# Optimization experiments

Measured on AMD Instinct MI355X. Metric: run time of the kernel, lower is better.

Reference implementation:

```python
import jax, jax.numpy as jnp
import numpy as np

B, N, M, C1, C2 = 4, 8192, 2048, 128, 256
H1, H2 = 256, 128  # mlp = [C2+C1, 256, 128]
EPS_DIST = 1e-8
EPS_BN = 1e-5
K = 3


def setup_inputs() -> dict:
    key = jax.random.key(0)
    ks = jax.random.split(key, 6)
    return {
        "unknown": jax.random.normal(ks[0], (B, N, 3), dtype=jnp.float32),
        "known": jax.random.normal(ks[1], (B, M, 3), dtype=jnp.float32),
        "unknow_feats": jax.random.normal(ks[2], (B, C1, N), dtype=jnp.float32),
        "known_feats": jax.random.normal(ks[3], (B, C2, M), dtype=jnp.float32),
        "W1": jax.random.normal(ks[4], (H1, C1 + C2), dtype=jnp.float32) * 0.05,
        "g1": jnp.ones((H1,), jnp.float32),
        "b1": jnp.zeros((H1,), jnp.float32),
        "W2": jax.random.normal(ks[5], (H2, H1), dtype=jnp.float32) * 0.05,
        "g2": jnp.ones((H2,), jnp.float32),
        "b2": jnp.zeros((H2,), jnp.float32),
    }


def _bn_relu(x, g, b):
    # training-mode BatchNorm over (batch, spatial) axes for (B, C, N) tensor
    mean = jnp.mean(x, axis=(0, 2), keepdims=True)
    var = jnp.var(x, axis=(0, 2), keepdims=True)
    y = (x - mean) * jax.lax.rsqrt(var + EPS_BN) * g[None, :, None] + b[None, :, None]
    return jax.nn.relu(y)


def reference(unknown, known, unknow_feats, known_feats, W1, g1, b1, W2, g2, b2):
    # 3-NN: squared euclidean distances (B, N, M) via expansion (avoids B,N,M,3 temp)
    d2 = (
        jnp.sum(unknown * unknown, axis=-1)[:, :, None]
        + jnp.sum(known * known, axis=-1)[:, None, :]
        - 2.0 * jnp.einsum("bnc,bmc->bnm", unknown, known)
    )
    neg_d, idx = jax.lax.top_k(-d2, K)  # smallest-K squared dists
    dist = -neg_d  # (B, N, K), squared distances (pytorch3d knn_points convention)
    recip = 1.0 / (dist + EPS_DIST)
    weight = recip / jnp.sum(recip, axis=2, keepdims=True)  # (B, N, K)

    kf = jnp.swapaxes(known_feats, 1, 2)  # (B, M, C2)
    grouped = jax.vmap(lambda f, i: f[i])(kf, idx)  # (B, N, K, C2)
    interp = jnp.einsum("bnkc,bnk->bcn", grouped, weight)  # (B, C2, N)

    x = jnp.concatenate([interp, unknow_feats], axis=1)  # (B, C2+C1, N)
    x = _bn_relu(jnp.einsum("oc,bcn->bon", W1, x), g1, b1)
    x = _bn_relu(jnp.einsum("oc,bcn->bon", W2, x), g2, b2)
    return x  # (B, H2, N)
```

## Files before the change

kernel.cpp:

```cpp
#include <hip/hip_runtime.h>
#include <hip/hip_bf16.h>
#include <cstdint>
#include <cstddef>

typedef unsigned short u16;
typedef __attribute__((ext_vector_type(8))) short bf16x8;
typedef __attribute__((ext_vector_type(4))) float f32x4;

constexpr int Bn = 4;
constexpr int Nq = 8192;
constexpr int Mk = 2048;
constexpr int C1c = 128;
constexpr int C2c = 256;
constexpr int H1c = 256;
constexpr int H2c = 128;

__device__ __forceinline__ float bf2f(u16 u) {
    union { uint32_t i; float f; } v;
    v.i = (uint32_t)u << 16;
    return v.f;
}
__device__ __forceinline__ u16 f2bf(float f) {
    const uint32_t x = __float_as_uint(f);
    return (u16)((x + 0x7FFFu + ((x >> 16) & 1u)) >> 16);
}
__device__ __forceinline__ uint32_t cvtpk(float lo, float hi) {
    uint32_t r;
    asm("v_cvt_pk_bf16_f32 %0, %1, %2" : "=v"(r) : "v"(lo), "v"(hi));
    return r;
}

__global__ __launch_bounds__(256) void knn_prep_kernel(
    const float* __restrict__ W1, const float* __restrict__ W2,
    u16* __restrict__ W1b, u16* __restrict__ W2b,
    const float* __restrict__ KF, u16* __restrict__ KFt,
    const float* __restrict__ UF, u16* __restrict__ UFt,
    const float* __restrict__ unknown, const float* __restrict__ known,
    int* __restrict__ idx_out, float* __restrict__ w_out)
{
    __shared__ __align__(16) char smem[32768];
    const int bid = blockIdx.x;
    const int t = threadIdx.x;

    if (bid < 2048) {
        float4* kp = (float4*)smem;
        const int b = bid >> 9;
        const int n0 = (bid & 511) * 16;

        const float* kb = known + (size_t)b * Mk * 3;
        for (int i = t; i < Mk; i += 256) {
            const float x = kb[i * 3 + 0], y = kb[i * 3 + 1], z = kb[i * 3 + 2];
            kp[i] = make_float4(x, y, z, fmaf(x, x, fmaf(y, y, z * z)));
        }
        __syncthreads();

        const int q = n0 + (t >> 4);
        const int s = t & 15;
        const float* u = unknown + ((size_t)b * Nq + q) * 3;
        const float ux = u[0], uy = u[1], uz = u[2];
        const float nux = -2.0f * ux, nuy = -2.0f * uy, nuz = -2.0f * uz;
        const float uu = fmaf(ux, ux, fmaf(uy, uy, uz * uz));

        float d0 = 1e30f, d1 = 1e30f, d2 = 1e30f;
        int i0 = 0, i1 = 0, i2 = 0;

        auto ins = [&](float d, int i) {
            const bool c0 = d < d0, c1 = d < d1, c2 = d < d2;
            const float nd0 = fminf(d0, d);
            const float nd1 = __builtin_amdgcn_fmed3f(d0, d, d1);
            const float nd2 = __builtin_amdgcn_fmed3f(d1, d, d2);
            i2 = c1 ? i1 : (c2 ? i : i2);
            i1 = c0 ? i0 : (c1 ? i : i1);
            i0 = c0 ? i : i0;
            d0 = nd0; d1 = nd1; d2 = nd2;
        };

        #pragma unroll 8
        for (int it = 0; it < Mk / 16; ++it) {
            const int m = it * 16 + s;
            const float4 p = kp[m];
            const float d = fmaf(nux, p.x, fmaf(nuy, p.y, fmaf(nuz, p.z, p.w)));
            ins(d, m);
        }
        #pragma unroll
        for (int off = 1; off <= 8; off <<= 1) {
            const float e0 = __shfl_xor(d0, off), e1 = __shfl_xor(d1, off), e2 = __shfl_xor(d2, off);
            const int j0 = __shfl_xor(i0, off), j1 = __shfl_xor(i1, off), j2 = __shfl_xor(i2, off);
            ins(e0, j0);
            ins(e1, j1);
            ins(e2, j2);
        }
        if (s == 0) {
            const float f0 = d0 + uu, f1 = d1 + uu, f2 = d2 + uu;
            const float r0 = 1.0f / (f0 + 1e-8f);
            const float r1 = 1.0f / (f1 + 1e-8f);
            const float r2 = 1.0f / (f2 + 1e-8f);
            const float inv = 1.0f / (r0 + r1 + r2);
            const size_t base = ((size_t)b * Nq + q) * 3;
            idx_out[base + 0] = i0;
            idx_out[base + 1] = i1;
            idx_out[base + 2] = i2;
            w_out[base + 0] = r0 * inv;
            w_out[base + 1] = r1 * inv;
            w_out[base + 2] = r2 * inv;
        }
    } else if (bid < 2176) {
        const int cb = bid - 2048;
        const float* X = (cb < 96) ? W1 : W2;
        u16* Y = (cb < 96) ? W1b : W2b;
        const int i = ((cb < 96) ? cb : (cb - 96)) * 256 + t;
        const float4 v = *(const float4*)&X[(size_t)i * 4];
        ushort4 o;
        o.x = f2bf(v.x); o.y = f2bf(v.y); o.z = f2bf(v.z); o.w = f2bf(v.w);
        *(ushort4*)&Y[(size_t)i * 4] = o;
    } else {
        const float* X;
        u16* Y;
        int C, M, m0, c0;
        if (bid < 2688) {
            const int f = bid - 2176;
            const int b = f >> 7, rem = f & 127;
            C = C2c; M = Mk; m0 = (rem >> 2) * 64; c0 = (rem & 3) * 64;
            X = KF + (size_t)b * C * M;
            Y = KFt + (size_t)b * M * C;
        } else {
            const int f = bid - 2688;
            const int b = f >> 8, rem = f & 255;
            C = C1c; M = Nq; m0 = (rem >> 1) * 64; c0 = (rem & 1) * 64;
            X = UF + (size_t)b * C * M;
            Y = UFt + (size_t)b * M * C;
        }
        float (*T)[65] = (float(*)[65])smem;
        const int m4 = (t & 15) * 4, cr = t >> 4;
        #pragma unroll
        for (int i = 0; i < 4; ++i) {
            const float4 v = *(const float4*)&X[(size_t)(c0 + cr + i * 16) * M + m0 + m4];
            T[cr + i * 16][m4 + 0] = v.x;
            T[cr + i * 16][m4 + 1] = v.y;
            T[cr + i * 16][m4 + 2] = v.z;
            T[cr + i * 16][m4 + 3] = v.w;
        }
        __syncthreads();
        const int c4 = (t & 15) * 4, mr = t >> 4;
        #pragma unroll
        for (int i = 0; i < 4; ++i) {
            const int m = mr + i * 16;
            ushort4 o;
            o.x = f2bf(T[c4 + 0][m]);
            o.y = f2bf(T[c4 + 1][m]);
            o.z = f2bf(T[c4 + 2][m]);
            o.w = f2bf(T[c4 + 3][m]);
            *(ushort4*)&Y[(size_t)(m0 + m) * C + c0 + c4] = o;
        }
    }
}

__device__ __forceinline__ uint4 bnx(uint4 x, const float* scs, const float* bis, int k) {
    const u16* p = (const u16*)&x;
    const float4 s0 = *(const float4*)&scs[k];
    const float4 s1 = *(const float4*)&scs[k + 4];
    const float4 b0 = *(const float4*)&bis[k];
    const float4 b1 = *(const float4*)&bis[k + 4];
    const float* sa = (const float*)&s0;
    const float* sb = (const float*)&s1;
    const float* ba = (const float*)&b0;
    const float* bb = (const float*)&b1;
    uint4 o;
    uint32_t* po = (uint32_t*)&o;
    #pragma unroll
    for (int w2 = 0; w2 < 2; ++w2) {
        const float a0 = fmaxf(0.0f, fmaf(bf2f(p[2 * w2 + 0]), sa[2 * w2 + 0], ba[2 * w2 + 0]));
        const float a1 = fmaxf(0.0f, fmaf(bf2f(p[2 * w2 + 1]), sa[2 * w2 + 1], ba[2 * w2 + 1]));
        po[w2] = cvtpk(a0, a1);
    }
    #pragma unroll
    for (int w2 = 0; w2 < 2; ++w2) {
        const float a0 = fmaxf(0.0f, fmaf(bf2f(p[4 + 2 * w2 + 0]), sb[2 * w2 + 0], bb[2 * w2 + 0]));
        const float a1 = fmaxf(0.0f, fmaf(bf2f(p[4 + 2 * w2 + 1]), sb[2 * w2 + 1], bb[2 * w2 + 1]));
        po[2 + w2] = cvtpk(a0, a1);
    }
    return o;
}

template <int GATHER, int OUT_BF16, int STATS, int BNIN>
__global__ __launch_bounds__(256) void mfma_gemm(
    const u16* __restrict__ A, int lda, size_t sA,
    const u16* __restrict__ Bt, int ldb, size_t sB,
    void* __restrict__ Cout, int ldc, size_t sC,
    int nK,
    const u16* __restrict__ Ptb,
    const int* __restrict__ idx, const float* __restrict__ wgt, int nrows,
    const float* __restrict__ bn_s, const float* __restrict__ bn_b,
    float* __restrict__ partS, float* __restrict__ partQ)
{
    __shared__ u16 As[4096];
    __shared__ u16 Bs[4096];
    __shared__ float scs[256], bis[256];
    __shared__ float sS[2][128], sQ[2][128];

    const int b = blockIdx.z;
    const int m0 = blockIdx.x * 128, n0 = blockIdx.y * 128;
    const int t = threadIdx.x;
    const int l = t & 63, wv = t >> 6;
    const int wr = wv >> 1, wc = wv & 1;

    if (BNIN) {
        scs[t] = bn_s[t];
        bis[t] = bn_b[t];
    }

    const u16* Ab = A + (size_t)b * sA;
    const u16* Btb = Bt + (size_t)b * sB;
    const int rA0 = t >> 2, rA1 = (t + 256) >> 2;
    const int ko = (t & 3) * 8;

    f32x4 acc[4][4];
    const f32x4 z = {0.0f, 0.0f, 0.0f, 0.0f};
    #pragma unroll
    for (int i = 0; i < 4; ++i)
        #pragma unroll
        for (int j = 0; j < 4; ++j) acc[i][j] = z;

    uint4 a0 = *(const uint4*)&Ab[(size_t)(m0 + rA0) * lda + ko];
    uint4 a1 = *(const uint4*)&Ab[(size_t)(m0 + rA1) * lda + ko];
    uint4 b0 = *(const uint4*)&Btb[(size_t)(n0 + rA0) * ldb + ko];
    uint4 b1 = *(const uint4*)&Btb[(size_t)(n0 + rA1) * ldb + ko];
    if (BNIN) __syncthreads();

    for (int kt = 0; kt < nK; ++kt) {
        *(uint4*)&As[t * 8] = a0;
        *(uint4*)&As[(t + 256) * 8] = a1;
        if (BNIN) {
            const int k = kt * 32 + ko;
            *(uint4*)&Bs[t * 8] = bnx(b0, scs, bis, k);
            *(uint4*)&Bs[(t + 256) * 8] = bnx(b1, scs, bis, k);
        } else {
            *(uint4*)&Bs[t * 8] = b0;
            *(uint4*)&Bs[(t + 256) * 8] = b1;
        }
        __syncthreads();
        if (kt + 1 < nK) {
            const int k0 = (kt + 1) * 32;
            a0 = *(const uint4*)&Ab[(size_t)(m0 + rA0) * lda + k0 + ko];
            a1 = *(const uint4*)&Ab[(size_t)(m0 + rA1) * lda + k0 + ko];
            b0 = *(const uint4*)&Btb[(size_t)(n0 + rA0) * ldb + k0 + ko];
            b1 = *(const uint4*)&Btb[(size_t)(n0 + rA1) * ldb + k0 + ko];
        }
        bf16x8 af[4], bf[4];
        #pragma unroll
        for (int f = 0; f < 4; ++f) {
            af[f] = *(const bf16x8*)&As[(wr * 64 + f * 16 + (l & 15)) * 32 + (l >> 4) * 8];
            bf[f] = *(const bf16x8*)&Bs[(wc * 64 + f * 16 + (l & 15)) * 32 + (l >> 4) * 8];
        }
        #pragma unroll
        for (int i = 0; i < 4; ++i)
            #pragma unroll
            for (int j = 0; j < 4; ++j)
                acc[i][j] = __builtin_amdgcn_mfma_f32_16x16x32_bf16(af[i], bf[j], acc[i][j], 0, 0, 0);
        __syncthreads();
    }

    const int cb = l & 15;
    const int rg = (l >> 4) * 4;
    float sj[4] = {0, 0, 0, 0}, qj[4] = {0, 0, 0, 0};
    #pragma unroll
    for (int i = 0; i < 4; ++i) {
        #pragma unroll
        for (int r = 0; r < 4; ++r) {
            const int R = m0 + wr * 64 + i * 16 + rg + r;
            const u16 *P0 = nullptr, *P1 = nullptr, *P2 = nullptr;
            float w0 = 0.0f, w1 = 0.0f, w2 = 0.0f;
            if (GATHER) {
                const size_t ib = ((size_t)b * nrows + R) * 3;
                const int j0 = idx[ib], j1 = idx[ib + 1], j2 = idx[ib + 2];
                w0 = wgt[ib];
                w1 = wgt[ib + 1];
                w2 = wgt[ib + 2];
                const u16* Pb = Ptb + (size_t)b * Mk * 256;
                P0 = Pb + (size_t)j0 * 256;
                P1 = Pb + (size_t)j1 * 256;
                P2 = Pb + (size_t)j2 * 256;
            }
            #pragma unroll
            for (int j = 0; j < 4; ++j) {
                const int Cc = n0 + wc * 64 + j * 16 + cb;
                float v = acc[i][j][r];
                if (GATHER)
                    v += w0 * bf2f(P0[Cc]) + w1 * bf2f(P1[Cc]) + w2 * bf2f(P2[Cc]);
                if (OUT_BF16)
                    ((u16*)Cout)[(size_t)b * sC + (size_t)R * ldc + Cc] = f2bf(v);
                else
                    ((float*)Cout)[(size_t)b * sC + (size_t)R * ldc + Cc] = v;
                if (STATS == 1) {
                    sj[j] += v;
                    qj[j] += v * v;
                }
                if (STATS == 2) acc[i][j][r] = v;
            }
        }
    }

    if (STATS == 1) {
        #pragma unroll
        for (int j = 0; j < 4; ++j) {
            float s = sj[j], q = qj[j];
            s += __shfl_xor(s, 16); s += __shfl_xor(s, 32);
            q += __shfl_xor(q, 16); q += __shfl_xor(q, 32);
            if (l < 16) {
                sS[wr][wc * 64 + j * 16 + l] = s;
                sQ[wr][wc * 64 + j * 16 + l] = q;
            }
        }
        __syncthreads();
        if (t < 128) {
            const float S = sS[0][t] + sS[1][t];
            const float Q = sQ[0][t] + sQ[1][t];
            const int pblk = blockIdx.z * gridDim.x + blockIdx.x;
            partS[(size_t)pblk * 256 + blockIdx.y * 128 + t] = S;
            partQ[(size_t)pblk * 256 + blockIdx.y * 128 + t] = Q;
        }
    }
    if (STATS == 2) {
        #pragma unroll
        for (int i = 0; i < 4; ++i) {
            #pragma unroll
            for (int r = 0; r < 4; ++r) {
                float s = acc[i][0][r] + acc[i][1][r] + acc[i][2][r] + acc[i][3][r];
                float q = acc[i][0][r] * acc[i][0][r] + acc[i][1][r] * acc[i][1][r] +
                          acc[i][2][r] * acc[i][2][r] + acc[i][3][r] * acc[i][3][r];
                s += __shfl_xor(s, 1); s += __shfl_xor(s, 2);
                s += __shfl_xor(s, 4); s += __shfl_xor(s, 8);
                q += __shfl_xor(q, 1); q += __shfl_xor(q, 2);
                q += __shfl_xor(q, 4); q += __shfl_xor(q, 8);
                if ((l & 15) == 0) {
                    const int row = wr * 64 + i * 16 + (l >> 4) * 4 + r;
                    sS[wc][row] = s;
                    sQ[wc][row] = q;
                }
            }
        }
        __syncthreads();
        if (t < 128) {
            const float S = sS[0][t] + sS[1][t];
            const float Q = sQ[0][t] + sQ[1][t];
            const int pblk = blockIdx.z * gridDim.y + blockIdx.y;
            partS[(size_t)pblk * 128 + t] = S;
            partQ[(size_t)pblk * 128 + t] = Q;
        }
    }
}

__global__ __launch_bounds__(1024) void bn_finalize(
    const float* __restrict__ pS, const float* __restrict__ pQ,
    const float* __restrict__ g, const float* __restrict__ beta,
    float* __restrict__ scale, float* __restrict__ bias,
    int C, int np, float cnt)
{
    __shared__ float rs[1024], rq[1024];
    const int t = threadIdx.x;
    const int c = t & (C - 1);
    const int sl = t / C;
    const int nsl = 1024 / C;
    float s = 0.0f, q = 0.0f;
    for (int i = sl; i < np; i += nsl) {
        s += pS[(size_t)i * C + c];
        q += pQ[(size_t)i * C + c];
    }
    rs[t] = s;
    rq[t] = q;
    __syncthreads();
    if (t < C) {
        for (int k = 1; k < nsl; ++k) {
            s += rs[t + k * C];
            q += rq[t + k * C];
        }
        const float mean = s / cnt;
        const float var = q / cnt - mean * mean;
        const float r = rsqrtf(var + 1e-5f);
        const float sc = g[t] * r;
        scale[t] = sc;
        bias[t] = beta[t] - mean * sc;
    }
}

__global__ __launch_bounds__(256) void bn2_apply_kernel(
    float* __restrict__ Y,
    const float* __restrict__ pS, const float* __restrict__ pQ,
    const float* __restrict__ g, const float* __restrict__ beta)
{
    __shared__ float rs[256], rq[256];
    const int t = threadIdx.x;
    const size_t base = (size_t)blockIdx.x * 1024;
    const int c = (int)((base / Nq) % H2c);

    rs[t] = pS[(size_t)t * 128 + c];
    rq[t] = pQ[(size_t)t * 128 + c];
    __syncthreads();
    for (int off = 128; off > 0; off >>= 1) {
        if (t < off) {
            rs[t] += rs[t + off];
            rq[t] += rq[t + off];
        }
        __syncthreads();
    }
    if (t == 0) {
        const float cnt = (float)(Bn * Nq);
        const float mean = rs[0] / cnt;
        const float var = rq[0] / cnt - mean * mean;
        const float r = rsqrtf(var + 1e-5f);
        const float sc = g[c] * r;
        rs[0] = sc;
        rq[0] = beta[c] - mean * sc;
    }
    __syncthreads();
    const float sc = rs[0], bi = rq[0];
    float4 v = *(float4*)&Y[base + t * 4];
    v.x = fmaxf(0.0f, fmaf(v.x, sc, bi));
    v.y = fmaxf(0.0f, fmaf(v.y, sc, bi));
    v.z = fmaxf(0.0f, fmaf(v.z, sc, bi));
    v.w = fmaxf(0.0f, fmaf(v.w, sc, bi));
    *(float4*)&Y[base + t * 4] = v;
}

extern "C" void kernel_launch(void* const* d_in, const int* in_sizes, int n_in,
                              void* d_out, int out_size, void* d_ws, size_t ws_size,
                              hipStream_t stream) {
    const float* unknown = (const float*)d_in[0];
    const float* known = (const float*)d_in[1];
    const float* unknow_feats = (const float*)d_in[2];
    const float* known_feats = (const float*)d_in[3];
    const float* W1 = (const float*)d_in[4];
    const float* g1 = (const float*)d_in[5];
    const float* b1 = (const float*)d_in[6];
    const float* W2 = (const float*)d_in[7];
    const float* g2 = (const float*)d_in[8];
    const float* b2 = (const float*)d_in[9];
    float* out = (float*)d_out;

    char* w = (char*)d_ws;
    u16* KFt = (u16*)w; w += (size_t)Bn * Mk * C2c * 2;
    u16* UFt = (u16*)w; w += (size_t)Bn * Nq * C1c * 2;
    u16* W1b = (u16*)w; w += (size_t)H1c * 384 * 2;
    u16* W2b = (u16*)w; w += (size_t)H2c * H1c * 2;
    u16* Ptb = (u16*)w; w += (size_t)Bn * Mk * H1c * 2;
    u16* y1b = (u16*)w; w += (size_t)Bn * Nq * H1c * 2;
    int* idx = (int*)w; w += (size_t)Bn * Nq * 3 * 4;
    float* wgt = (float*)w; w += (size_t)Bn * Nq * 3 * 4;
    float* pS1 = (float*)w; w += (size_t)256 * 256 * 4;
    float* pQ1 = (float*)w; w += (size_t)256 * 256 * 4;
    float* pS2 = (float*)w; w += (size_t)256 * 128 * 4;
    float* pQ2 = (float*)w; w += (size_t)256 * 128 * 4;
    float* scale1 = (float*)w; w += 1024;
    float* bias1 = (float*)w; w += 1024;

    knn_prep_kernel<<<3712, 256, 0, stream>>>(W1, W2, W1b, W2b,
                                              known_feats, KFt, unknow_feats, UFt,
                                              unknown, known, idx, wgt);

    mfma_gemm<0, 1, 0, 0><<<dim3(Mk / 128, H1c / 128, Bn), 256, 0, stream>>>(
        KFt, C2c, (size_t)Mk * C2c,
        W1b, 384, 0,
        Ptb, H1c, (size_t)Mk * H1c,
        C2c / 32, nullptr, nullptr, nullptr, 0,
        nullptr, nullptr, nullptr, nullptr);

    mfma_gemm<1, 1, 1, 0><<<dim3(Nq / 128, H1c / 128, Bn), 256, 0, stream>>>(
        UFt, C1c, (size_t)Nq * C1c,
        W1b + C2c, 384, 0,
        y1b, H1c, (size_t)Nq * H1c,
        C1c / 32, Ptb, idx, wgt, Nq,
        nullptr, nullptr, pS1, pQ1);

    bn_finalize<<<1, 1024, 0, stream>>>(pS1, pQ1, g1, b1, scale1, bias1,
                                        H1c, 256, (float)(Bn * Nq));

    mfma_gemm<0, 0, 2, 1><<<dim3(1, Nq / 128, Bn), 256, 0, stream>>>(
        W2b, H1c, 0,
        y1b, H1c, (size_t)Nq * H1c,
        out, Nq, (size_t)H2c * Nq,
        H1c / 32, nullptr, nullptr, nullptr, 0,
        scale1, bias1, pS2, pQ2);

    bn2_apply_kernel<<<(Bn * H2c * Nq) / 1024, 256, 0, stream>>>(out, pS2, pQ2, g2, b2);
}
```

Before: 109.2 us.

## Fuse known-feature projection into prep kernel, pair-split KNN scan, split GEMM3 tiles

The known_feats transpose plus separate MFMA GEMM for the W1 projection is replaced by an FP32 SIMT tiled GEMM inside the prep kernel, which writes Ptb directly and removes one launch and the KFt buffer. The KNN scan now handles two candidates per iteration, sorting the pair first and inserting the larger one with a cheaper partial insert; the shuffle merge also uses reduced insert variants. The templated GEMM is split into specialised kernels, and the final GEMM uses 64-row tiles over a grid twice as large for more parallelism. The FP32 SIMT projection is slower per flop than MFMA and may lengthen the prep kernel's critical path.

```diff
diff --git a/kernel.cpp b/kernel.cpp
--- a/kernel.cpp
+++ b/kernel.cpp
@@ -33,7 +33,7 @@
 __global__ __launch_bounds__(256) void knn_prep_kernel(
     const float* __restrict__ W1, const float* __restrict__ W2,
     u16* __restrict__ W1b, u16* __restrict__ W2b,
-    const float* __restrict__ KF, u16* __restrict__ KFt,
+    const float* __restrict__ KF, u16* __restrict__ Ptb,
     const float* __restrict__ UF, u16* __restrict__ UFt,
     const float* __restrict__ unknown, const float* __restrict__ known,
     int* __restrict__ idx_out, float* __restrict__ w_out)
@@ -74,21 +74,41 @@
             i0 = c0 ? i : i0;
             d0 = nd0; d1 = nd1; d2 = nd2;
         };
-
-        #pragma unroll 8
-        for (int it = 0; it < Mk / 16; ++it) {
-            const int m = it * 16 + s;
-            const float4 p = kp[m];
-            const float d = fmaf(nux, p.x, fmaf(nuy, p.y, fmaf(nuz, p.z, p.w)));
-            ins(d, m);
+        auto ins_hi = [&](float d, int i) {
+            const bool c1 = d < d1, c2 = d < d2;
+            const float nd1 = fminf(d1, d);
+            const float nd2 = __builtin_amdgcn_fmed3f(d1, d, d2);
+            i2 = c1 ? i1 : (c2 ? i : i2);
+            i1 = c1 ? i : i1;
+            d1 = nd1; d2 = nd2;
+        };
+        auto ins_top = [&](float d, int i) {
+            const bool c2 = d < d2;
+            d2 = fminf(d2, d);
+            i2 = c2 ? i : i2;
+        };
+
+        #pragma unroll 4
+        for (int it = 0; it < Mk / 32; ++it) {
+            const int ma = it * 16 + s;
+            const int mb = ma + 1024;
+            const float4 pa = kp[ma];
+            const float4 pb = kp[mb];
+            const float da = fmaf(nux, pa.x, fmaf(nuy, pa.y, fmaf(nuz, pa.z, pa.w)));
+            const float db = fmaf(nux, pb.x, fmaf(nuy, pb.y, fmaf(nuz, pb.z, pb.w)));
+            const bool cab = da < db;
+            const float dlo = fminf(da, db), dhi = fmaxf(da, db);
+            const int ilo = cab ? ma : mb, ihi = cab ? mb : ma;
+            ins(dlo, ilo);
+            ins_hi(dhi, ihi);
         }
         #pragma unroll
         for (int off = 1; off <= 8; off <<= 1) {
             const float e0 = __shfl_xor(d0, off), e1 = __shfl_xor(d1, off), e2 = __shfl_xor(d2, off);
             const int j0 = __shfl_xor(i0, off), j1 = __shfl_xor(i1, off), j2 = __shfl_xor(i2, off);
             ins(e0, j0);
-            ins(e1, j1);
-            ins(e2, j2);
+            ins_hi(e1, j1);
+            ins_top(e2, j2);
         }
         if (s == 0) {
             const float f0 = d0 + uu, f1 = d1 + uu, f2 = d2 + uu;
@@ -104,8 +124,59 @@
             w_out[base + 1] = r1 * inv;
             w_out[base + 2] = r2 * inv;
         }
-    } else if (bid < 2176) {
-        const int cb = bid - 2048;
+    } else if (bid < 2304) {
+        float (*Xs)[128] = (float(*)[128])smem;
+        float (*Ws)[65] = (float(*)[65])(smem + 8192);
+        const int f = bid - 2048;
+        const int b = f >> 6;
+        const int rem = f & 63;
+        const int m0 = (rem >> 2) * 128;
+        const int h0 = (rem & 3) * 64;
+        const float* Xb = KF + (size_t)b * C2c * Mk;
+        const int tx = t & 15, ty = t >> 4;
+
+        float acc[8][4] = {};
+        for (int k0 = 0; k0 < C2c; k0 += 16) {
+            {
+                const int mx = (t & 31) * 4, kx = t >> 5;
+                #pragma unroll
+                for (int i = 0; i < 2; ++i)
+                    *(float4*)&Xs[kx + i * 8][mx] =
+                        *(const float4*)&Xb[(size_t)(k0 + kx + i * 8) * Mk + m0 + mx];
+            }
+            {
+                const int kw = t & 15, hw = t >> 4;
+                #pragma unroll
+                for (int i = 0; i < 4; ++i)
+                    Ws[kw][hw + i * 16] = W1[(size_t)(h0 + hw + i * 16) * 384 + k0 + kw];
+            }
+            __syncthreads();
+            #pragma unroll
+            for (int k = 0; k < 16; ++k) {
+                float a[8], bv[4];
+                *(float4*)&a[0] = *(const float4*)&Xs[k][ty * 8];
+                *(float4*)&a[4] = *(const float4*)&Xs[k][ty * 8 + 4];
+                *(float4*)&bv[0] = *(const float4*)&Ws[k][tx * 4];
+                #pragma unroll
+                for (int i = 0; i < 8; ++i)
+                    #pragma unroll
+                    for (int j = 0; j < 4; ++j)
+                        acc[i][j] = fmaf(a[i], bv[j], acc[i][j]);
+            }
+            __syncthreads();
+        }
+        u16* Yb = Ptb + (size_t)b * Mk * 256;
+        #pragma unroll
+        for (int i = 0; i < 8; ++i) {
+            ushort4 o;
+            o.x = f2bf(acc[i][0]);
+            o.y = f2bf(acc[i][1]);
+            o.z = f2bf(acc[i][2]);
+            o.w = f2bf(acc[i][3]);
+            *(ushort4*)&Yb[(size_t)(m0 + ty * 8 + i) * 256 + h0 + tx * 4] = o;
+        }
+    } else if (bid < 2432) {
+        const int cb = bid - 2304;
         const float* X = (cb < 96) ? W1 : W2;
         u16* Y = (cb < 96) ? W1b : W2b;
         const int i = ((cb < 96) ? cb : (cb - 96)) * 256 + t;
@@ -114,27 +185,16 @@
         o.x = f2bf(v.x); o.y = f2bf(v.y); o.z = f2bf(v.z); o.w = f2bf(v.w);
         *(ushort4*)&Y[(size_t)i * 4] = o;
     } else {
-        const float* X;
-        u16* Y;
-        int C, M, m0, c0;
-        if (bid < 2688) {
-            const int f = bid - 2176;
-            const int b = f >> 7, rem = f & 127;
-            C = C2c; M = Mk; m0 = (rem >> 2) * 64; c0 = (rem & 3) * 64;
-            X = KF + (size_t)b * C * M;
-            Y = KFt + (size_t)b * M * C;
-        } else {
-            const int f = bid - 2688;
-            const int b = f >> 8, rem = f & 255;
-            C = C1c; M = Nq; m0 = (rem >> 1) * 64; c0 = (rem & 1) * 64;
-            X = UF + (size_t)b * C * M;
-            Y = UFt + (size_t)b * M * C;
-        }
+        const int f = bid - 2432;
+        const int b = f >> 8, rem = f & 255;
+        const int m0 = (rem >> 1) * 64, c0 = (rem & 1) * 64;
+        const float* X = UF + (size_t)b * C1c * Nq;
+        u16* Y = UFt + (size_t)b * Nq * C1c;
         float (*T)[65] = (float(*)[65])smem;
         const int m4 = (t & 15) * 4, cr = t >> 4;
         #pragma unroll
         for (int i = 0; i < 4; ++i) {
-            const float4 v = *(const float4*)&X[(size_t)(c0 + cr + i * 16) * M + m0 + m4];
+            const float4 v = *(const float4*)&X[(size_t)(c0 + cr + i * 16) * Nq + m0 + m4];
             T[cr + i * 16][m4 + 0] = v.x;
             T[cr + i * 16][m4 + 1] = v.y;
             T[cr + i * 16][m4 + 2] = v.z;
@@ -150,7 +210,7 @@
             o.y = f2bf(T[c4 + 1][m]);
             o.z = f2bf(T[c4 + 2][m]);
             o.w = f2bf(T[c4 + 3][m]);
-            *(ushort4*)&Y[(size_t)(m0 + m) * C + c0 + c4] = o;
+            *(ushort4*)&Y[(size_t)(m0 + m) * C1c + c0 + c4] = o;
         }
     }
 }
@@ -182,20 +242,17 @@
     return o;
 }
 
-template <int GATHER, int OUT_BF16, int STATS, int BNIN>
-__global__ __launch_bounds__(256) void mfma_gemm(
+__global__ __launch_bounds__(256) void mfma_gemm2(
     const u16* __restrict__ A, int lda, size_t sA,
-    const u16* __restrict__ Bt, int ldb, size_t sB,
-    void* __restrict__ Cout, int ldc, size_t sC,
+    const u16* __restrict__ Bt, int ldb,
+    u16* __restrict__ Cout,
     int nK,
     const u16* __restrict__ Ptb,
-    const int* __restrict__ idx, const float* __restrict__ wgt, int nrows,
-    const float* __restrict__ bn_s, const float* __restrict__ bn_b,
+    const int* __restrict__ idx, const float* __restrict__ wgt,
     float* __restrict__ partS, float* __restrict__ partQ)
 {
     __shared__ u16 As[4096];
     __shared__ u16 Bs[4096];
-    __shared__ float scs[256], bis[256];
     __shared__ float sS[2][128], sQ[2][128];
 
     const int b = blockIdx.z;
@@ -204,13 +261,7 @@
     const int l = t & 63, wv = t >> 6;
     const int wr = wv >> 1, wc = wv & 1;
 
-    if (BNIN) {
-        scs[t] = bn_s[t];
-        bis[t] = bn_b[t];
-    }
-
     const u16* Ab = A + (size_t)b * sA;
-    const u16* Btb = Bt + (size_t)b * sB;
     const int rA0 = t >> 2, rA1 = (t + 256) >> 2;
     const int ko = (t & 3) * 8;
 
@@ -223,28 +274,21 @@
 
     uint4 a0 = *(const uint4*)&Ab[(size_t)(m0 + rA0) * lda + ko];
     uint4 a1 = *(const uint4*)&Ab[(size_t)(m0 + rA1) * lda + ko];
-    uint4 b0 = *(const uint4*)&Btb[(size_t)(n0 + rA0) * ldb + ko];
-    uint4 b1 = *(const uint4*)&Btb[(size_t)(n0 + rA1) * ldb + ko];
-    if (BNIN) __syncthreads();
+    uint4 b0 = *(const uint4*)&Bt[(size_t)(n0 + rA0) * ldb + ko];
+    uint4 b1 = *(const uint4*)&Bt[(size_t)(n0 + rA1) * ldb + ko];
 
     for (int kt = 0; kt < nK; ++kt) {
         *(uint4*)&As[t * 8] = a0;
         *(uint4*)&As[(t + 256) * 8] = a1;
-        if (BNIN) {
-            const int k = kt * 32 + ko;
-            *(uint4*)&Bs[t * 8] = bnx(b0, scs, bis, k);
-            *(uint4*)&Bs[(t + 256) * 8] = bnx(b1, scs, bis, k);
-        } else {
-            *(uint4*)&Bs[t * 8] = b0;
-            *(uint4*)&Bs[(t + 256) * 8] = b1;
-        }
+        *(uint4*)&Bs[t * 8] = b0;
+        *(uint4*)&Bs[(t + 256) * 8] = b1;
         __syncthreads();
         if (kt + 1 < nK) {
             const int k0 = (kt + 1) * 32;
             a0 = *(const uint4*)&Ab[(size_t)(m0 + rA0) * lda + k0 + ko];
             a1 = *(const uint4*)&Ab[(size_t)(m0 + rA1) * lda + k0 + ko];
-            b0 = *(const uint4*)&Btb[(size_t)(n0 + rA0) * ldb + k0 + ko];
-            b1 = *(const uint4*)&Btb[(size_t)(n0 + rA1) * ldb + k0 + ko];
+            b0 = *(const uint4*)&Bt[(size_t)(n0 + rA0) * ldb + k0 + ko];
+            b1 = *(const uint4*)&Bt[(size_t)(n0 + rA1) * ldb + k0 + ko];
         }
         bf16x8 af[4], bf[4];
         #pragma unroll
@@ -268,85 +312,144 @@
         #pragma unroll
         for (int r = 0; r < 4; ++r) {
             const int R = m0 + wr * 64 + i * 16 + rg + r;
-            const u16 *P0 = nullptr, *P1 = nullptr, *P2 = nullptr;
-            float w0 = 0.0f, w1 = 0.0f, w2 = 0.0f;
-            if (GATHER) {
-                const size_t ib = ((size_t)b * nrows + R) * 3;
-                const int j0 = idx[ib], j1 = idx[ib + 1], j2 = idx[ib + 2];
-                w0 = wgt[ib];
-                w1 = wgt[ib + 1];
-                w2 = wgt[ib + 2];
-                const u16* Pb = Ptb + (size_t)b * Mk * 256;
-                P0 = Pb + (size_t)j0 * 256;
-                P1 = Pb + (size_t)j1 * 256;
-                P2 = Pb + (size_t)j2 * 256;
-            }
+            const size_t ib = ((size_t)b * Nq + R) * 3;
+            const int j0 = idx[ib], j1 = idx[ib + 1], j2 = idx[ib + 2];
+            const float w0 = wgt[ib], w1 = wgt[ib + 1], w2 = wgt[ib + 2];
+            const u16* Pb = Ptb + (size_t)b * Mk * 256;
+            const u16* P0 = Pb + (size_t)j0 * 256;
+            const u16* P1 = Pb + (size_t)j1 * 256;
+            const u16* P2 = Pb + (size_t)j2 * 256;
             #pragma unroll
             for (int j = 0; j < 4; ++j) {
                 const int Cc = n0 + wc * 64 + j * 16 + cb;
                 float v = acc[i][j][r];
-                if (GATHER)
-                    v += w0 * bf2f(P0[Cc]) + w1 * bf2f(P1[Cc]) + w2 * bf2f(P2[Cc]);
-                if (OUT_BF16)
-                    ((u16*)Cout)[(size_t)b * sC + (size_t)R * ldc + Cc] = f2bf(v);
-                else
-                    ((float*)Cout)[(size_t)b * sC + (size_t)R * ldc + Cc] = v;
-                if (STATS == 1) {
-                    sj[j] += v;
-                    qj[j] += v * v;
-                }
-                if (STATS == 2) acc[i][j][r] = v;
+                v += w0 * bf2f(P0[Cc]) + w1 * bf2f(P1[Cc]) + w2 * bf2f(P2[Cc]);
+                Cout[(size_t)b * Nq * 256 + (size_t)R * 256 + Cc] = f2bf(v);
+                sj[j] += v;
+                qj[j] += v * v;
             }
         }
     }
 
-    if (STATS == 1) {
-        #pragma unroll
-        for (int j = 0; j < 4; ++j) {
-            float s = sj[j], q = qj[j];
-            s += __shfl_xor(s, 16); s += __shfl_xor(s, 32);
-            q += __shfl_xor(q, 16); q += __shfl_xor(q, 32);
-            if (l < 16) {
-                sS[wr][wc * 64 + j * 16 + l] = s;
-                sQ[wr][wc * 64 + j * 16 + l] = q;
+    #pragma unroll
+    for (int j = 0; j < 4; ++j) {
+        float s = sj[j], q = qj[j];
+        s += __shfl_xor(s, 16); s += __shfl_xor(s, 32);
+        q += __shfl_xor(q, 16); q += __shfl_xor(q, 32);
+        if (l < 16) {
+            sS[wr][wc * 64 + j * 16 + l] = s;
+            sQ[wr][wc * 64 + j * 16 + l] = q;
+        }
+    }
+    __syncthreads();
+    if (t < 128) {
+        const float S = sS[0][t] + sS[1][t];
+        const float Q = sQ[0][t] + sQ[1][t];
+        const int pblk = blockIdx.z * gridDim.x + blockIdx.x;
+        partS[(size_t)pblk * 256 + blockIdx.y * 128 + t] = S;
+        partQ[(size_t)pblk * 256 + blockIdx.y * 128 + t] = Q;
+    }
+}
+
+__global__ __launch_bounds__(256) void mfma_gemm3(
+    const u16* __restrict__ W2b,
+    const u16* __restrict__ Y,
+    float* __restrict__ out,
+    const float* __restrict__ bn_s, const float* __restrict__ bn_b,
+    float* __restrict__ partS, float* __restrict__ partQ)
+{
+    __shared__ u16 As[2048];
+    __shared__ u16 Bs[4096];
+    __shared__ float scs[256], bis[256];
+    __shared__ float sS[2][64], sQ[2][64];
+
+    const int b = blockIdx.z;
+    const int m0 = blockIdx.x * 64;
+    const int n0 = blockIdx.y * 128;
+    const int t = threadIdx.x;
+    const int l = t & 63, wv = t >> 6;
+    const int wr = wv >> 1, wc = wv & 1;
+
+    scs[t] = bn_s[t];
+    bis[t] = bn_b[t];
+
+    const u16* Yb = Y + (size_t)b * Nq * 256;
+    const int rA = t >> 2;
+    const int rB1 = (t + 256) >> 2;
+    const int ko = (t & 3) * 8;
+
+    f32x4 acc[2][4];
+    const f32x4 z = {0.0f, 0.0f, 0.0f, 0.0f};
+    #pragma unroll
+    for (int i = 0; i < 2; ++i)
+        #pragma unroll
+        for (int j = 0; j < 4; ++j) acc[i][j] = z;
+
+    uint4 a0 = *(const uint4*)&W2b[(size_t)(m0 + rA) * 256 + ko];
+    uint4 b0 = *(const uint4*)&Yb[(size_t)(n0 + rA) * 256 + ko];
+    uint4 b1 = *(const uint4*)&Yb[(size_t)(n0 + rB1) * 256 + ko];
+    __syncthreads();
+
+    for (int kt = 0; kt < 8; ++kt) {
+        const int k = kt * 32 + ko;
+        *(uint4*)&As[t * 8] = a0;
+        *(uint4*)&Bs[t * 8] = bnx(b0, scs, bis, k);
+        *(uint4*)&Bs[(t + 256) * 8] = bnx(b1, scs, bis, k);
+        __syncthreads();
+        if (kt + 1 < 8) {
+            const int k0 = (kt + 1) * 32;
+            a0 = *(const uint4*)&W2b[(size_t)(m0 + rA) * 256 + k0 + ko];
+            b0 = *(const uint4*)&Yb[(size_t)(n0 + rA) * 256 + k0 + ko];
+            b1 = *(const uint4*)&Yb[(size_t)(n0 + rB1) * 256 + k0 + ko];
+        }
+        bf16x8 af[2], bf[4];
+        #pragma unroll
+        for (int f = 0; f < 2; ++f)
+            af[f] = *(const bf16x8*)&As[(wr * 32 + f * 16 + (l & 15)) * 32 + (l >> 4) * 8];
+        #pragma unroll
+        for (int f = 0; f < 4; ++f)
+            bf[f] = *(const bf16x8*)&Bs[(wc * 64 + f * 16 + (l & 15)) * 32 + (l >> 4) * 8];
+        #pragma unroll
+        for (int i = 0; i < 2; ++i)
+            #pragma unroll
+            for (int j = 0; j < 4; ++j)
+                acc[i][j] = __builtin_amdgcn_mfma_f32_16x16x32_bf16(af[i], bf[j], acc[i][j], 0, 0, 0);
+        __syncthreads();
+    }
+
+    const int cb = l & 15;
+    const int rg = (l >> 4) * 4;
+    float* ob = out + (size_t)b * H2c * Nq;
+    #pragma unroll
+    for (int i = 0; i < 2; ++i) {
+        #pragma unroll
+        for (int r = 0; r < 4; ++r) {
+            const int Rl = wr * 32 + i * 16 + rg + r;
+            #pragma unroll
+            for (int j = 0; j < 4; ++j) {
+                const int Cc = n0 + wc * 64 + j * 16 + cb;
+                ob[(size_t)(m0 + Rl) * Nq + Cc] = acc[i][j][r];
             }
-        }
-        __syncthreads();
-        if (t < 128) {
-            const float S = sS[0][t] + sS[1][t];
-            const float Q = sQ[0][t] + sQ[1][t];
-            const int pblk = blockIdx.z * gridDim.x + blockIdx.x;
-            partS[(size_t)pblk * 256 + blockIdx.y * 128 + t] = S;
-            partQ[(size_t)pblk * 256 + blockIdx.y * 128 + t] = Q;
-        }
-    }
-    if (STATS == 2) {
-        #pragma unroll
-        for (int i = 0; i < 4; ++i) {
-            #pragma unroll
-            for (int r = 0; r < 4; ++r) {
-                float s = acc[i][0][r] + acc[i][1][r] + acc[i][2][r] + acc[i][3][r];
-                float q = acc[i][0][r] * acc[i][0][r] + acc[i][1][r] * acc[i][1][r] +
-                          acc[i][2][r] * acc[i][2][r] + acc[i][3][r] * acc[i][3][r];
-                s += __shfl_xor(s, 1); s += __shfl_xor(s, 2);
-                s += __shfl_xor(s, 4); s += __shfl_xor(s, 8);
-                q += __shfl_xor(q, 1); q += __shfl_xor(q, 2);
-                q += __shfl_xor(q, 4); q += __shfl_xor(q, 8);
-                if ((l & 15) == 0) {
-                    const int row = wr * 64 + i * 16 + (l >> 4) * 4 + r;
-                    sS[wc][row] = s;
-                    sQ[wc][row] = q;
-                }
+            float s = acc[i][0][r] + acc[i][1][r] + acc[i][2][r] + acc[i][3][r];
+            float q = acc[i][0][r] * acc[i][0][r] + acc[i][1][r] * acc[i][1][r] +
+                      acc[i][2][r] * acc[i][2][r] + acc[i][3][r] * acc[i][3][r];
+            s += __shfl_xor(s, 1); s += __shfl_xor(s, 2);
+            s += __shfl_xor(s, 4); s += __shfl_xor(s, 8);
+            q += __shfl_xor(q, 1); q += __shfl_xor(q, 2);
+            q += __shfl_xor(q, 4); q += __shfl_xor(q, 8);
+            if ((l & 15) == 0) {
+                sS[wc][Rl] = s;
+                sQ[wc][Rl] = q;
             }
         }
-        __syncthreads();
-        if (t < 128) {
-            const float S = sS[0][t] + sS[1][t];
-            const float Q = sQ[0][t] + sQ[1][t];
-            const int pblk = blockIdx.z * gridDim.y + blockIdx.y;
-            partS[(size_t)pblk * 128 + t] = S;
-            partQ[(size_t)pblk * 128 + t] = Q;
-        }
+    }
+    __syncthreads();
+    if (t < 64) {
+        const float S = sS[0][t] + sS[1][t];
+        const float Q = sQ[0][t] + sQ[1][t];
+        const int p = blockIdx.z * gridDim.y + blockIdx.y;
+        partS[(size_t)p * 128 + m0 + t] = S;
+        partQ[(size_t)p * 128 + m0 + t] = Q;
     }
 }
 
@@ -438,7 +541,6 @@
     float* out = (float*)d_out;
 
     char* w = (char*)d_ws;
-    u16* KFt = (u16*)w; w += (size_t)Bn * Mk * C2c * 2;
     u16* UFt = (u16*)w; w += (size_t)Bn * Nq * C1c * 2;
     u16* W1b = (u16*)w; w += (size_t)H1c * 384 * 2;
     u16* W2b = (u16*)w; w += (size_t)H2c * H1c * 2;
@@ -453,33 +555,21 @@
     float* scale1 = (float*)w; w += 1024;
     float* bias1 = (float*)w; w += 1024;
 
-    knn_prep_kernel<<<3712, 256, 0, stream>>>(W1, W2, W1b, W2b,
-                                              known_feats, KFt, unknow_feats, UFt,
+    knn_prep_kernel<<<3456, 256, 0, stream>>>(W1, W2, W1b, W2b,
+                                              known_feats, Ptb, unknow_feats, UFt,
                                               unknown, known, idx, wgt);
 
-    mfma_gemm<0, 1, 0, 0><<<dim3(Mk / 128, H1c / 128, Bn), 256, 0, stream>>>(
-        KFt, C2c, (size_t)Mk * C2c,
-        W1b, 384, 0,
-        Ptb, H1c, (size_t)Mk * H1c,
-        C2c / 32, nullptr, nullptr, nullptr, 0,
-        nullptr, nullptr, nullptr, nullptr);
-
-    mfma_gemm<1, 1, 1, 0><<<dim3(Nq / 128, H1c / 128, Bn), 256, 0, stream>>>(
+    mfma_gemm2<<<dim3(Nq / 128, H1c / 128, Bn), 256, 0, stream>>>(
         UFt, C1c, (size_t)Nq * C1c,
-        W1b + C2c, 384, 0,
-        y1b, H1c, (size_t)Nq * H1c,
-        C1c / 32, Ptb, idx, wgt, Nq,
-        nullptr, nullptr, pS1, pQ1);
+        W1b + C2c, 384,
+        y1b, C1c / 32,
+        Ptb, idx, wgt, pS1, pQ1);
 
     bn_finalize<<<1, 1024, 0, stream>>>(pS1, pQ1, g1, b1, scale1, bias1,
                                         H1c, 256, (float)(Bn * Nq));
 
-    mfma_gemm<0, 0, 2, 1><<<dim3(1, Nq / 128, Bn), 256, 0, stream>>>(
-        W2b, H1c, 0,
-        y1b, H1c, (size_t)Nq * H1c,
-        out, Nq, (size_t)H2c * Nq,
-        H1c / 32, nullptr, nullptr, nullptr, 0,
-        scale1, bias1, pS2, pQ2);
+    mfma_gemm3<<<dim3(2, Nq / 128, Bn), 256, 0, stream>>>(
+        W2b, y1b, out, scale1, bias1, pS2, pQ2);
 
     bn2_apply_kernel<<<(Bn * H2c * Nq) / 1024, 256, 0, stream>>>(out, pS2, pQ2, g2, b2);
 }
```

Measured after the change: 129.9 us. +19.0%, slower.
